# Kernel tuning notes

Hardware: AMD Instinct MI355X
Metric: run time of the kernel (lower is better)

Reference implementation:

```python
import jax, jax.numpy as jnp
import numpy as np
from jax import lax

EPS = 1e-5
B, C, H, W = 64, 32, 128, 128

def _bn(x, gamma, beta, mean, var):
    # inference-mode batchnorm over channel dim (NCHW)
    scale = gamma / jnp.sqrt(var + EPS)
    return x * scale[None, :, None, None] + (beta - mean * scale)[None, :, None, None]

def _conv3x3(x, w, b):
    # 3x3 conv, stride 1, padding 1, NCHW / OIHW
    y = lax.conv_general_dilated(x, w, window_strides=(1, 1), padding=((1, 1), (1, 1)),
                                 dimension_numbers=('NCHW', 'OIHW', 'NCHW'))
    return y + b[None, :, None, None]


def setup_inputs() -> dict:
    key = jax.random.key(0)
    ks = jax.random.split(key, 13)
    fan_in = C * 9
    return {
        'x': jax.random.normal(ks[0], (B, C, H, W), jnp.float32),
        'bn1_gamma': jax.random.uniform(ks[1], (C,), jnp.float32, 0.5, 1.5),
        'bn1_beta': jax.random.normal(ks[2], (C,), jnp.float32) * 0.1,
        'bn1_mean': jax.random.normal(ks[3], (C,), jnp.float32) * 0.1,
        'bn1_var': jax.random.uniform(ks[4], (C,), jnp.float32, 0.5, 1.5),
        'w1': jax.random.normal(ks[5], (C, C, 3, 3), jnp.float32) / np.sqrt(fan_in),
        'b1': jax.random.normal(ks[6], (C,), jnp.float32) * 0.01,
        'bn2_gamma': jax.random.uniform(ks[7], (C,), jnp.float32, 0.5, 1.5),
        'bn2_beta': jax.random.normal(ks[8], (C,), jnp.float32) * 0.1,
        'bn2_mean': jax.random.normal(ks[9], (C,), jnp.float32) * 0.1,
        'bn2_var': jax.random.uniform(ks[10], (C,), jnp.float32, 0.5, 1.5),
        'w2': jax.random.normal(ks[11], (C, C, 3, 3), jnp.float32) / np.sqrt(fan_in),
        'b2': jax.random.normal(ks[12], (C,), jnp.float32) * 0.01,
    }


def reference(x, bn1_gamma, bn1_beta, bn1_mean, bn1_var, w1, b1,
              bn2_gamma, bn2_beta, bn2_mean, bn2_var, w2, b2):
    # BN -> ReLU -> conv3x3 -> (dropout: identity in eval) -> BN -> ReLU -> conv3x3
    h = jnp.maximum(_bn(x, bn1_gamma, bn1_beta, bn1_mean, bn1_var), 0.0)
    h = _conv3x3(h, w1, b1)
    h = jnp.maximum(_bn(h, bn2_gamma, bn2_beta, bn2_mean, bn2_var), 0.0)
    h = _conv3x3(h, w2, b2)
    # stride=1 and in_channels==channels -> identity shortcut
    return h + x
```

## Files before the change

kernel.cpp:

```cpp
#include <hip/hip_runtime.h>

#define EPSV 1e-5f

typedef __bf16 bf16x8 __attribute__((ext_vector_type(8)));
typedef float f32x4 __attribute__((ext_vector_type(4)));
typedef float f32x2 __attribute__((ext_vector_type(2)));
typedef unsigned short ushort8 __attribute__((ext_vector_type(8)));

__global__ __launch_bounds__(256) void prep_weights(
    const float* __restrict__ w1, const float* __restrict__ b1,
    const float* __restrict__ g2, const float* __restrict__ be2,
    const float* __restrict__ m2, const float* __restrict__ v2,
    const float* __restrict__ w2,
    const float* __restrict__ g1, const float* __restrict__ be1,
    const float* __restrict__ m1, const float* __restrict__ v1,
    __bf16* __restrict__ wf1, __bf16* __restrict__ wf2,
    float* __restrict__ bias1p, float* __restrict__ sc1, float* __restrict__ sf1) {
  int i = blockIdx.x * 256 + threadIdx.x;
  int conv = i / 9216;
  int rem  = i % 9216;
  int tap  = rem >> 10;
  int r2   = rem & 1023;
  int half = r2 >> 9;
  int lane = (r2 >> 3) & 63;
  int j    = r2 & 7;
  int ci = ((lane >> 4) << 3) + j;
  int co = half * 16 + (lane & 15);
  float val = (conv ? w2 : w1)[(co * 32 + ci) * 9 + tap];
  if (!conv) val *= g2[co] * rsqrtf(v2[co] + EPSV);
  (conv ? wf2 : wf1)[rem] = (__bf16)val;
  if (blockIdx.x == 0 && threadIdx.x < 32) {
    int c = threadIdx.x;
    float s2 = g2[c] * rsqrtf(v2[c] + EPSV);
    bias1p[c] = s2 * b1[c] + (be2[c] - m2[c] * s2);
  }
  if (blockIdx.x == 0 && threadIdx.x >= 64 && threadIdx.x < 96) {
    int c = threadIdx.x - 64;
    float s = g1[c] * rsqrtf(v1[c] + EPSV);
    sc1[c] = s;
    sf1[c] = be1[c] - m1[c] * s;
  }
}

__global__ __launch_bounds__(256, 2) void bnconv1(
    const float* __restrict__ x,
    const float* __restrict__ sc1, const float* __restrict__ sf1,
    const __bf16* __restrict__ wfrag, const float* __restrict__ bias,
    unsigned short* __restrict__ outb) {
  __shared__ __align__(16) unsigned short tile[6 * 4160];
  char* tb = reinterpret_cast<char*>(tile);
  int t = threadIdx.x, lane = t & 63, wv = t >> 6;
  int Bw = blockIdx.x;
  int logical = (Bw & 7) * 256 + (Bw >> 3);
  int b = logical >> 5, h0 = (logical & 31) * 4;

  float sc[8], sf[8];
  #pragma unroll
  for (int cc = 0; cc < 8; cc++) { sc[cc] = sc1[wv * 8 + cc]; sf[cc] = sf1[wv * 8 + cc]; }

  int wbyte0 = (2 * lane + 1) * 64 + ((wv ^ (lane & 3)) << 4);
  #pragma unroll
  for (int k = 0; k < 6; k++) {
    int hr = h0 - 1 + k;
    char* dst = tb + k * 8320 + wbyte0;
    if (hr >= 0 && hr < 128) {
      const float* src = x + (long)(b * 32 + wv * 8) * 16384 + hr * 128 + 2 * lane;
      float p0[8], p1[8];
      #pragma unroll
      for (int cc = 0; cc < 8; cc++) {
        f32x2 v = *reinterpret_cast<const f32x2*>(src + cc * 16384);
        p0[cc] = fmaxf(fmaf(v[0], sc[cc], sf[cc]), 0.0f);
        p1[cc] = fmaxf(fmaf(v[1], sc[cc], sf[cc]), 0.0f);
      }
      bf16x8 a0, a1;
      #pragma unroll
      for (int cc = 0; cc < 8; cc++) { a0[cc] = (__bf16)p0[cc]; a1[cc] = (__bf16)p1[cc]; }
      *reinterpret_cast<bf16x8*>(dst) = a0;
      *reinterpret_cast<bf16x8*>(dst + 64) = a1;
    } else {
      *reinterpret_cast<bf16x8*>(dst) = bf16x8{};
      *reinterpret_cast<bf16x8*>(dst + 64) = bf16x8{};
    }
  }
  if (t < 48) {
    int sl = t >> 3, r2 = t & 7;
    int phys = (r2 >> 2) * 129, ch = r2 & 3;
    *reinterpret_cast<ushort8*>(&tile[sl * 4160 + phys * 32 + ch * 8]) = ushort8{};
  }

  bf16x8 Bf[9][2];
  #pragma unroll
  for (int tap = 0; tap < 9; tap++)
    #pragma unroll
    for (int hf = 0; hf < 2; hf++)
      Bf[tap][hf] = reinterpret_cast<const bf16x8*>(wfrag)[(tap * 2 + hf) * 64 + lane];
  float bco[2] = { bias[lane & 15], bias[16 + (lane & 15)] };

  int cb = lane >> 4;
  int offs[2][3];
  #pragma unroll
  for (int g = 0; g < 2; g++)
    #pragma unroll
    for (int dx = 0; dx < 3; dx++) {
      int w = wv * 32 + g * 16 + (lane & 15) + dx - 1;
      int s = cb ^ ((w >> 1) & 3);
      offs[g][dx] = (w + 1) * 64 + s * 16;
    }

  __syncthreads();

  f32x4 acc4[4][2][2] = {};
  #pragma unroll
  for (int r = 0; r < 4; r++)
    #pragma unroll
    for (int dy = 0; dy < 3; dy++) {
      const char* rowbase = tb + (r + dy) * 8320;
      #pragma unroll
      for (int dx = 0; dx < 3; dx++)
        #pragma unroll
        for (int g = 0; g < 2; g++) {
          bf16x8 a = *reinterpret_cast<const bf16x8*>(rowbase + offs[g][dx]);
          acc4[r][g][0] = __builtin_amdgcn_mfma_f32_16x16x32_bf16(a, Bf[dy * 3 + dx][0], acc4[r][g][0], 0, 0, 0);
          acc4[r][g][1] = __builtin_amdgcn_mfma_f32_16x16x32_bf16(a, Bf[dy * 3 + dx][1], acc4[r][g][1], 0, 0, 0);
        }
    }

  __syncthreads();
  #pragma unroll
  for (int r = 0; r < 4; r++)
    #pragma unroll
    for (int g = 0; g < 2; g++)
      #pragma unroll
      for (int hf = 0; hf < 2; hf++) {
        int co = hf * 16 + (lane & 15);
        #pragma unroll
        for (int j = 0; j < 4; j++) {
          int pix = wv * 32 + g * 16 + ((lane >> 4) << 2) + j;
          float val = fmaxf(acc4[r][g][hf][j] + bco[hf], 0.0f);
          int byte = r * 8192 + pix * 64 + (((co >> 3) ^ ((pix >> 1) & 3)) << 4) + (co & 7) * 2;
          *reinterpret_cast<unsigned short*>(tb + byte) =
              __builtin_bit_cast(unsigned short, (__bf16)val);
        }
      }
  __syncthreads();
  unsigned short* dst = outb + ((long)(b * 128 + h0) * 128) * 32;
  #pragma unroll
  for (int i = 0; i < 8; i++) {
    int u = i * 256 + t;
    *reinterpret_cast<ushort8*>(dst + u * 8) =
        *reinterpret_cast<const ushort8*>(tb + u * 16);
  }
}

__global__ __launch_bounds__(256, 2) void conv2_direct(
    const unsigned short* __restrict__ hb,
    const __bf16* __restrict__ wfrag, const float* __restrict__ bias,
    const float* __restrict__ xres, float* __restrict__ outf) {
  int t = threadIdx.x, lane = t & 63, wv = t >> 6;
  int Bw = blockIdx.x;
  int logical = (Bw & 7) * 256 + (Bw >> 3);
  int b = logical >> 5, h0 = (logical & 31) * 4;

  bf16x8 Bf[9][2];
  #pragma unroll
  for (int tap = 0; tap < 9; tap++)
    #pragma unroll
    for (int hf = 0; hf < 2; hf++)
      Bf[tap][hf] = reinterpret_cast<const bf16x8*>(wfrag)[(tap * 2 + hf) * 64 + lane];
  float bco[2] = { bias[lane & 15], bias[16 + (lane & 15)] };

  int cb = lane >> 4;
  int coloff[2][3];
  bool colbad[2][3];
  #pragma unroll
  for (int g = 0; g < 2; g++)
    #pragma unroll
    for (int dx = 0; dx < 3; dx++) {
      int w = wv * 32 + g * 16 + (lane & 15) + dx - 1;
      colbad[g][dx] = (w < 0) || (w > 127);
      int wc = w < 0 ? 0 : (w > 127 ? 127 : w);
      int s = cb ^ ((wc >> 1) & 3);
      coloff[g][dx] = wc * 64 + s * 16;
    }

  const char* hbase = reinterpret_cast<const char*>(hb) + (long)b * 128 * 8192;

  #pragma unroll
  for (int r = 0; r < 4; r++) {
    f32x4 acc[2][2] = {};
    #pragma unroll
    for (int dy = 0; dy < 3; dy++) {
      int hr_in = h0 + r + dy - 1;
      if (hr_in >= 0 && hr_in < 128) {
        const char* rowb = hbase + (long)hr_in * 8192;
        #pragma unroll
        for (int dx = 0; dx < 3; dx++)
          #pragma unroll
          for (int g = 0; g < 2; g++) {
            bf16x8 a = *reinterpret_cast<const bf16x8*>(rowb + coloff[g][dx]);
            if (colbad[g][dx]) a = bf16x8{};
            acc[g][0] = __builtin_amdgcn_mfma_f32_16x16x32_bf16(a, Bf[dy * 3 + dx][0], acc[g][0], 0, 0, 0);
            acc[g][1] = __builtin_amdgcn_mfma_f32_16x16x32_bf16(a, Bf[dy * 3 + dx][1], acc[g][1], 0, 0, 0);
          }
      }
    }
    int hr = h0 + r;
    #pragma unroll
    for (int g = 0; g < 2; g++)
      #pragma unroll
      for (int hf = 0; hf < 2; hf++) {
        int co = hf * 16 + (lane & 15);
        int pix0 = wv * 32 + g * 16 + ((lane >> 4) << 2);
        long idx = ((long)(b * 32 + co) * 128 + hr) * 128 + pix0;
        f32x4 xr = *reinterpret_cast<const f32x4*>(xres + idx);
        f32x4 o;
        #pragma unroll
        for (int j = 0; j < 4; j++) o[j] = acc[g][hf][j] + bco[hf] + xr[j];
        *reinterpret_cast<f32x4*>(outf + idx) = o;
      }
  }
}

extern "C" void kernel_launch(void* const* d_in, const int* in_sizes, int n_in,
                              void* d_out, int out_size, void* d_ws, size_t ws_size,
                              hipStream_t stream) {
  const float* x   = (const float*)d_in[0];
  const float* g1  = (const float*)d_in[1];
  const float* be1 = (const float*)d_in[2];
  const float* m1  = (const float*)d_in[3];
  const float* v1  = (const float*)d_in[4];
  const float* w1  = (const float*)d_in[5];
  const float* b1  = (const float*)d_in[6];
  const float* g2  = (const float*)d_in[7];
  const float* be2 = (const float*)d_in[8];
  const float* m2  = (const float*)d_in[9];
  const float* v2  = (const float*)d_in[10];
  const float* w2  = (const float*)d_in[11];
  const float* b2  = (const float*)d_in[12];

  char* ws = (char*)d_ws;
  unsigned short* hb = (unsigned short*)ws;
  __bf16* wf1    = (__bf16*)(ws + 67108864);
  __bf16* wf2    = (__bf16*)(ws + 67108864 + 18432);
  float*  bias1p = (float*)(ws + 67108864 + 36864);
  float*  sc1    = (float*)(ws + 67108864 + 36992);
  float*  sf1    = (float*)(ws + 67108864 + 37120);

  prep_weights<<<dim3(72), dim3(256), 0, stream>>>(
      w1, b1, g2, be2, m2, v2, w2, g1, be1, m1, v1, wf1, wf2, bias1p, sc1, sf1);
  bnconv1<<<dim3(2048), dim3(256), 0, stream>>>(x, sc1, sf1, wf1, bias1p, hb);
  conv2_direct<<<dim3(2048), dim3(256), 0, stream>>>(hb, wf2, b2, x, (float*)d_out);
}
```

Measured before the change: 326.7 us.

## Fuse both convolutions into one kernel with halo recompute in LDS

Merges the BN+conv1 and conv2 kernels into one kernel that loads an 8-row input halo, computes the six needed conv1 rows (including halo rows) into a rolling LDS buffer, and runs conv2 directly from LDS. This removes the 64MB bf16 intermediate write and read through global memory and one kernel launch. In exchange it recomputes halo rows (6 conv1 rows per 4 output rows), adds more barriers, and keeps both weight sets live, with conv2 weights reloaded per tap, which may raise register pressure.

```diff
diff --git a/kernel.cpp b/kernel.cpp
--- a/kernel.cpp
+++ b/kernel.cpp
@@ -42,27 +42,49 @@
   }
 }
 
-__global__ __launch_bounds__(256, 2) void bnconv1(
+__global__ __launch_bounds__(256, 2) void fused_conv(
     const float* __restrict__ x,
     const float* __restrict__ sc1, const float* __restrict__ sf1,
-    const __bf16* __restrict__ wfrag, const float* __restrict__ bias,
-    unsigned short* __restrict__ outb) {
-  __shared__ __align__(16) unsigned short tile[6 * 4160];
+    const __bf16* __restrict__ wf1, const __bf16* __restrict__ wf2,
+    const float* __restrict__ bias1p, const float* __restrict__ b2,
+    float* __restrict__ outf) {
+  __shared__ __align__(16) unsigned short tile[8 * 4096];
   char* tb = reinterpret_cast<char*>(tile);
   int t = threadIdx.x, lane = t & 63, wv = t >> 6;
   int Bw = blockIdx.x;
   int logical = (Bw & 7) * 256 + (Bw >> 3);
   int b = logical >> 5, h0 = (logical & 31) * 4;
 
+  bf16x8 Bf1[9][2];
+  #pragma unroll
+  for (int tap = 0; tap < 9; tap++)
+    #pragma unroll
+    for (int hf = 0; hf < 2; hf++)
+      Bf1[tap][hf] = reinterpret_cast<const bf16x8*>(wf1)[(tap * 2 + hf) * 64 + lane];
+  float bco1[2] = { bias1p[lane & 15], bias1p[16 + (lane & 15)] };
+  float bco2[2] = { b2[lane & 15], b2[16 + (lane & 15)] };
+
+  int cb = lane >> 4;
+  int offs[2][3];
+  bool bad[2][3];
+  #pragma unroll
+  for (int g = 0; g < 2; g++)
+    #pragma unroll
+    for (int dx = 0; dx < 3; dx++) {
+      int w = wv * 32 + g * 16 + (lane & 15) + dx - 1;
+      bad[g][dx] = (w < 0) || (w > 127);
+      int wc = w < 0 ? 0 : (w > 127 ? 127 : w);
+      offs[g][dx] = wc * 64 + ((cb ^ ((wc >> 1) & 3)) << 4);
+    }
+
   float sc[8], sf[8];
   #pragma unroll
   for (int cc = 0; cc < 8; cc++) { sc[cc] = sc1[wv * 8 + cc]; sf[cc] = sf1[wv * 8 + cc]; }
-
-  int wbyte0 = (2 * lane + 1) * 64 + ((wv ^ (lane & 3)) << 4);
-  #pragma unroll
-  for (int k = 0; k < 6; k++) {
-    int hr = h0 - 1 + k;
-    char* dst = tb + k * 8320 + wbyte0;
+  int wb0 = 128 * lane + ((wv ^ (lane & 3)) << 4);
+  #pragma unroll
+  for (int k = 0; k < 8; k++) {
+    int hr = h0 - 2 + k;
+    char* dst = tb + k * 8192 + wb0;
     if (hr >= 0 && hr < 128) {
       const float* src = x + (long)(b * 32 + wv * 8) * 16384 + hr * 128 + 2 * lane;
       float p0[8], p1[8];
@@ -82,142 +104,145 @@
       *reinterpret_cast<bf16x8*>(dst + 64) = bf16x8{};
     }
   }
-  if (t < 48) {
-    int sl = t >> 3, r2 = t & 7;
-    int phys = (r2 >> 2) * 129, ch = r2 & 3;
-    *reinterpret_cast<ushort8*>(&tile[sl * 4160 + phys * 32 + ch * 8]) = ushort8{};
-  }
-
-  bf16x8 Bf[9][2];
-  #pragma unroll
-  for (int tap = 0; tap < 9; tap++)
-    #pragma unroll
-    for (int hf = 0; hf < 2; hf++)
-      Bf[tap][hf] = reinterpret_cast<const bf16x8*>(wfrag)[(tap * 2 + hf) * 64 + lane];
-  float bco[2] = { bias[lane & 15], bias[16 + (lane & 15)] };
-
-  int cb = lane >> 4;
-  int offs[2][3];
-  #pragma unroll
-  for (int g = 0; g < 2; g++)
-    #pragma unroll
-    for (int dx = 0; dx < 3; dx++) {
-      int w = wv * 32 + g * 16 + (lane & 15) + dx - 1;
-      int s = cb ^ ((w >> 1) & 3);
-      offs[g][dx] = (w + 1) * 64 + s * 16;
-    }
-
   __syncthreads();
 
-  f32x4 acc4[4][2][2] = {};
-  #pragma unroll
-  for (int r = 0; r < 4; r++)
+  f32x4 ha[3][2][2] = {};
+  #pragma unroll
+  for (int m = -1; m <= 1; m++) {
+    if (h0 + m >= 0) {
+      #pragma unroll
+      for (int dy = 0; dy < 3; dy++) {
+        const char* rb = tb + (m + 1 + dy) * 8192;
+        #pragma unroll
+        for (int dx = 0; dx < 3; dx++)
+          #pragma unroll
+          for (int g = 0; g < 2; g++) {
+            bf16x8 a = *reinterpret_cast<const bf16x8*>(rb + offs[g][dx]);
+            if (bad[g][dx]) a = bf16x8{};
+            ha[m + 1][g][0] = __builtin_amdgcn_mfma_f32_16x16x32_bf16(a, Bf1[dy * 3 + dx][0], ha[m + 1][g][0], 0, 0, 0);
+            ha[m + 1][g][1] = __builtin_amdgcn_mfma_f32_16x16x32_bf16(a, Bf1[dy * 3 + dx][1], ha[m + 1][g][1], 0, 0, 0);
+          }
+      }
+    }
+  }
+  __syncthreads();
+  #pragma unroll
+  for (int m = -1; m <= 1; m++) {
+    if (h0 + m >= 0) {
+      #pragma unroll
+      for (int g = 0; g < 2; g++)
+        #pragma unroll
+        for (int hf = 0; hf < 2; hf++) {
+          int co = hf * 16 + (lane & 15);
+          #pragma unroll
+          for (int j = 0; j < 4; j++) {
+            int pix = wv * 32 + g * 16 + ((lane >> 4) << 2) + j;
+            float val = fmaxf(ha[m + 1][g][hf][j] + bco1[hf], 0.0f);
+            int byte = (m + 1) * 8192 + pix * 64 + (((co >> 3) ^ ((pix >> 1) & 3)) << 4) + (co & 7) * 2;
+            *reinterpret_cast<unsigned short*>(tb + byte) =
+                __builtin_bit_cast(unsigned short, (__bf16)val);
+          }
+        }
+    } else {
+      char* zb = tb + (m + 1) * 8192 + t * 32;
+      *reinterpret_cast<ushort8*>(zb) = ushort8{};
+      *reinterpret_cast<ushort8*>(zb + 16) = ushort8{};
+    }
+  }
+  __syncthreads();
+
+  #pragma unroll
+  for (int r = 0; r < 4; r++) {
+    f32x4 c2[2][2] = {};
     #pragma unroll
     for (int dy = 0; dy < 3; dy++) {
-      const char* rowbase = tb + (r + dy) * 8320;
-      #pragma unroll
-      for (int dx = 0; dx < 3; dx++)
+      const char* rb = tb + (r + dy) * 8192;
+      #pragma unroll
+      for (int dx = 0; dx < 3; dx++) {
+        bf16x8 B0 = reinterpret_cast<const bf16x8*>(wf2)[((dy * 3 + dx) * 2 + 0) * 64 + lane];
+        bf16x8 B1 = reinterpret_cast<const bf16x8*>(wf2)[((dy * 3 + dx) * 2 + 1) * 64 + lane];
         #pragma unroll
         for (int g = 0; g < 2; g++) {
-          bf16x8 a = *reinterpret_cast<const bf16x8*>(rowbase + offs[g][dx]);
-          acc4[r][g][0] = __builtin_amdgcn_mfma_f32_16x16x32_bf16(a, Bf[dy * 3 + dx][0], acc4[r][g][0], 0, 0, 0);
-          acc4[r][g][1] = __builtin_amdgcn_mfma_f32_16x16x32_bf16(a, Bf[dy * 3 + dx][1], acc4[r][g][1], 0, 0, 0);
-        }
-    }
-
-  __syncthreads();
-  #pragma unroll
-  for (int r = 0; r < 4; r++)
-    #pragma unroll
-    for (int g = 0; g < 2; g++)
-      #pragma unroll
-      for (int hf = 0; hf < 2; hf++) {
-        int co = hf * 16 + (lane & 15);
-        #pragma unroll
-        for (int j = 0; j < 4; j++) {
-          int pix = wv * 32 + g * 16 + ((lane >> 4) << 2) + j;
-          float val = fmaxf(acc4[r][g][hf][j] + bco[hf], 0.0f);
-          int byte = r * 8192 + pix * 64 + (((co >> 3) ^ ((pix >> 1) & 3)) << 4) + (co & 7) * 2;
-          *reinterpret_cast<unsigned short*>(tb + byte) =
-              __builtin_bit_cast(unsigned short, (__bf16)val);
-        }
-      }
-  __syncthreads();
-  unsigned short* dst = outb + ((long)(b * 128 + h0) * 128) * 32;
-  #pragma unroll
-  for (int i = 0; i < 8; i++) {
-    int u = i * 256 + t;
-    *reinterpret_cast<ushort8*>(dst + u * 8) =
-        *reinterpret_cast<const ushort8*>(tb + u * 16);
-  }
-}
-
-__global__ __launch_bounds__(256, 2) void conv2_direct(
-    const unsigned short* __restrict__ hb,
-    const __bf16* __restrict__ wfrag, const float* __restrict__ bias,
-    const float* __restrict__ xres, float* __restrict__ outf) {
-  int t = threadIdx.x, lane = t & 63, wv = t >> 6;
-  int Bw = blockIdx.x;
-  int logical = (Bw & 7) * 256 + (Bw >> 3);
-  int b = logical >> 5, h0 = (logical & 31) * 4;
-
-  bf16x8 Bf[9][2];
-  #pragma unroll
-  for (int tap = 0; tap < 9; tap++)
-    #pragma unroll
-    for (int hf = 0; hf < 2; hf++)
-      Bf[tap][hf] = reinterpret_cast<const bf16x8*>(wfrag)[(tap * 2 + hf) * 64 + lane];
-  float bco[2] = { bias[lane & 15], bias[16 + (lane & 15)] };
-
-  int cb = lane >> 4;
-  int coloff[2][3];
-  bool colbad[2][3];
-  #pragma unroll
-  for (int g = 0; g < 2; g++)
-    #pragma unroll
-    for (int dx = 0; dx < 3; dx++) {
-      int w = wv * 32 + g * 16 + (lane & 15) + dx - 1;
-      colbad[g][dx] = (w < 0) || (w > 127);
-      int wc = w < 0 ? 0 : (w > 127 ? 127 : w);
-      int s = cb ^ ((wc >> 1) & 3);
-      coloff[g][dx] = wc * 64 + s * 16;
-    }
-
-  const char* hbase = reinterpret_cast<const char*>(hb) + (long)b * 128 * 8192;
-
-  #pragma unroll
-  for (int r = 0; r < 4; r++) {
-    f32x4 acc[2][2] = {};
-    #pragma unroll
-    for (int dy = 0; dy < 3; dy++) {
-      int hr_in = h0 + r + dy - 1;
-      if (hr_in >= 0 && hr_in < 128) {
-        const char* rowb = hbase + (long)hr_in * 8192;
-        #pragma unroll
-        for (int dx = 0; dx < 3; dx++)
-          #pragma unroll
-          for (int g = 0; g < 2; g++) {
-            bf16x8 a = *reinterpret_cast<const bf16x8*>(rowb + coloff[g][dx]);
-            if (colbad[g][dx]) a = bf16x8{};
-            acc[g][0] = __builtin_amdgcn_mfma_f32_16x16x32_bf16(a, Bf[dy * 3 + dx][0], acc[g][0], 0, 0, 0);
-            acc[g][1] = __builtin_amdgcn_mfma_f32_16x16x32_bf16(a, Bf[dy * 3 + dx][1], acc[g][1], 0, 0, 0);
-          }
-      }
-    }
-    int hr = h0 + r;
-    #pragma unroll
-    for (int g = 0; g < 2; g++)
-      #pragma unroll
-      for (int hf = 0; hf < 2; hf++) {
-        int co = hf * 16 + (lane & 15);
-        int pix0 = wv * 32 + g * 16 + ((lane >> 4) << 2);
-        long idx = ((long)(b * 32 + co) * 128 + hr) * 128 + pix0;
-        f32x4 xr = *reinterpret_cast<const f32x4*>(xres + idx);
-        f32x4 o;
-        #pragma unroll
-        for (int j = 0; j < 4; j++) o[j] = acc[g][hf][j] + bco[hf] + xr[j];
-        *reinterpret_cast<f32x4*>(outf + idx) = o;
-      }
+          bf16x8 a = *reinterpret_cast<const bf16x8*>(rb + offs[g][dx]);
+          if (bad[g][dx]) a = bf16x8{};
+          c2[g][0] = __builtin_amdgcn_mfma_f32_16x16x32_bf16(a, B0, c2[g][0], 0, 0, 0);
+          c2[g][1] = __builtin_amdgcn_mfma_f32_16x16x32_bf16(a, B1, c2[g][1], 0, 0, 0);
+        }
+      }
+    }
+
+    if (r < 3) {
+      f32x4 hn[2][2] = {};
+      bool inimg = (h0 + r + 2) < 128;
+      if (inimg) {
+        #pragma unroll
+        for (int dy = 0; dy < 3; dy++) {
+          const char* rb = tb + (r + 3 + dy) * 8192;
+          #pragma unroll
+          for (int dx = 0; dx < 3; dx++)
+            #pragma unroll
+            for (int g = 0; g < 2; g++) {
+              bf16x8 a = *reinterpret_cast<const bf16x8*>(rb + offs[g][dx]);
+              if (bad[g][dx]) a = bf16x8{};
+              hn[g][0] = __builtin_amdgcn_mfma_f32_16x16x32_bf16(a, Bf1[dy * 3 + dx][0], hn[g][0], 0, 0, 0);
+              hn[g][1] = __builtin_amdgcn_mfma_f32_16x16x32_bf16(a, Bf1[dy * 3 + dx][1], hn[g][1], 0, 0, 0);
+            }
+        }
+      }
+      {
+        int hr = h0 + r;
+        #pragma unroll
+        for (int g = 0; g < 2; g++)
+          #pragma unroll
+          for (int hf = 0; hf < 2; hf++) {
+            int co = hf * 16 + (lane & 15);
+            int pix0 = wv * 32 + g * 16 + ((lane >> 4) << 2);
+            long idx = ((long)(b * 32 + co) * 128 + hr) * 128 + pix0;
+            f32x4 xr = *reinterpret_cast<const f32x4*>(x + idx);
+            f32x4 o;
+            #pragma unroll
+            for (int j = 0; j < 4; j++) o[j] = c2[g][hf][j] + bco2[hf] + xr[j];
+            *reinterpret_cast<f32x4*>(outf + idx) = o;
+          }
+      }
+      __syncthreads();
+      if (inimg) {
+        #pragma unroll
+        for (int g = 0; g < 2; g++)
+          #pragma unroll
+          for (int hf = 0; hf < 2; hf++) {
+            int co = hf * 16 + (lane & 15);
+            #pragma unroll
+            for (int j = 0; j < 4; j++) {
+              int pix = wv * 32 + g * 16 + ((lane >> 4) << 2) + j;
+              float val = fmaxf(hn[g][hf][j] + bco1[hf], 0.0f);
+              int byte = (r + 3) * 8192 + pix * 64 + (((co >> 3) ^ ((pix >> 1) & 3)) << 4) + (co & 7) * 2;
+              *reinterpret_cast<unsigned short*>(tb + byte) =
+                  __builtin_bit_cast(unsigned short, (__bf16)val);
+            }
+          }
+      } else {
+        char* zb = tb + (r + 3) * 8192 + t * 32;
+        *reinterpret_cast<ushort8*>(zb) = ushort8{};
+        *reinterpret_cast<ushort8*>(zb + 16) = ushort8{};
+      }
+      __syncthreads();
+    } else {
+      int hr = h0 + r;
+      #pragma unroll
+      for (int g = 0; g < 2; g++)
+        #pragma unroll
+        for (int hf = 0; hf < 2; hf++) {
+          int co = hf * 16 + (lane & 15);
+          int pix0 = wv * 32 + g * 16 + ((lane >> 4) << 2);
+          long idx = ((long)(b * 32 + co) * 128 + hr) * 128 + pix0;
+          f32x4 xr = *reinterpret_cast<const f32x4*>(x + idx);
+          f32x4 o;
+          #pragma unroll
+          for (int j = 0; j < 4; j++) o[j] = c2[g][hf][j] + bco2[hf] + xr[j];
+          *reinterpret_cast<f32x4*>(outf + idx) = o;
+        }
+    }
   }
 }
 
@@ -239,15 +264,14 @@
   const float* b2  = (const float*)d_in[12];
 
   char* ws = (char*)d_ws;
-  unsigned short* hb = (unsigned short*)ws;
-  __bf16* wf1    = (__bf16*)(ws + 67108864);
-  __bf16* wf2    = (__bf16*)(ws + 67108864 + 18432);
-  float*  bias1p = (float*)(ws + 67108864 + 36864);
-  float*  sc1    = (float*)(ws + 67108864 + 36992);
-  float*  sf1    = (float*)(ws + 67108864 + 37120);
+  __bf16* wf1    = (__bf16*)ws;
+  __bf16* wf2    = (__bf16*)(ws + 18432);
+  float*  bias1p = (float*)(ws + 36864);
+  float*  sc1    = (float*)(ws + 36992);
+  float*  sf1    = (float*)(ws + 37120);
 
   prep_weights<<<dim3(72), dim3(256), 0, stream>>>(
       w1, b1, g2, be2, m2, v2, w2, g1, be1, m1, v1, wf1, wf2, bias1p, sc1, sf1);
-  bnconv1<<<dim3(2048), dim3(256), 0, stream>>>(x, sc1, sf1, wf1, bias1p, hb);
-  conv2_direct<<<dim3(2048), dim3(256), 0, stream>>>(hb, wf2, b2, x, (float*)d_out);
+  fused_conv<<<dim3(2048), dim3(256), 0, stream>>>(
+      x, sc1, sf1, wf1, wf2, bias1p, b2, (float*)d_out);
 }
```

Result: faster. 308.1 us (-5.7%).
